# Optimization experiments

Measured on AMD Instinct MI355X. Metric: run time of the kernel, lower is better.

The kernel has to match this reference:

```python
import jax, jax.numpy as jnp
import numpy as np

N = 16384
D_IN = 1024
HID = [512, 512, 256]
N_PAIRS = 100000
N_CLS = 3


def setup_inputs() -> dict:
    key = jax.random.key(0)
    ks = jax.random.split(key, 16)
    x = jax.random.normal(ks[0], (N, D_IN), dtype=jnp.float32)
    adj = jax.random.uniform(ks[1], (N, N), dtype=jnp.float32) / N  # dense normalized adjacency
    tf_idx = jax.random.randint(ks[2], (N_PAIRS,), 0, N)
    gene_idx = jax.random.randint(ks[3], (N_PAIRS,), 0, N)
    # GCN layer weights
    W0 = jax.random.normal(ks[4], (D_IN, HID[0]), dtype=jnp.float32) / np.sqrt(D_IN)
    b0 = jnp.zeros((HID[0],), dtype=jnp.float32)
    W1 = jax.random.normal(ks[5], (HID[0], HID[1]), dtype=jnp.float32) / np.sqrt(HID[0])
    b1 = jnp.zeros((HID[1],), dtype=jnp.float32)
    W2 = jax.random.normal(ks[6], (HID[1], HID[2]), dtype=jnp.float32) / np.sqrt(HID[1])
    b2 = jnp.zeros((HID[2],), dtype=jnp.float32)
    # MLP head: Linear(2*256 -> 256), GELU, Linear(256 -> 3)
    Wh1 = jax.random.normal(ks[7], (2 * HID[2], HID[2]), dtype=jnp.float32) / np.sqrt(2 * HID[2])
    bh1 = jnp.zeros((HID[2],), dtype=jnp.float32)
    Wh2 = jax.random.normal(ks[8], (HID[2], N_CLS), dtype=jnp.float32) / np.sqrt(HID[2])
    bh2 = jnp.zeros((N_CLS,), dtype=jnp.float32)
    return {"x": x, "adj": adj, "tf_idx": tf_idx, "gene_idx": gene_idx,
            "W0": W0, "b0": b0, "W1": W1, "b1": b1, "W2": W2, "b2": b2,
            "Wh1": Wh1, "bh1": bh1, "Wh2": Wh2, "bh2": bh2}


def reference(x, adj, tf_idx, gene_idx, W0, b0, W1, b1, W2, b2, Wh1, bh1, Wh2, bh2):
    # GCNConv: out = adj @ (x @ W) + b; ReLU between layers (dropout off in eval)
    h = jax.nn.relu(adj @ (x @ W0) + b0)          # [N, 512]
    h = jax.nn.relu(adj @ (h @ W1) + b1)          # [N, 512]
    emb = adj @ (h @ W2) + b2                      # [N, 256]
    pair = jnp.concatenate([emb[tf_idx], emb[gene_idx]], axis=-1)  # [P, 512]
    hdn = jax.nn.gelu(pair @ Wh1 + bh1, approximate=False)          # [P, 256]
    logits = hdn @ Wh2 + bh2                                        # [P, 3]
    return logits
```

## Files before the change

### kernel.cpp

```cpp
#include <hip/hip_runtime.h>
#include <hip/hip_bf16.h>
#include <stdint.h>


using f32x4  = __attribute__((ext_vector_type(4))) float;
using bf16x8 = __attribute__((ext_vector_type(8))) __bf16;
using u16x8  = __attribute__((ext_vector_type(8))) unsigned short;
using u16x4  = __attribute__((ext_vector_type(4))) unsigned short;

static __device__ __forceinline__ unsigned short f2bf(float f) {
  unsigned u = __builtin_bit_cast(unsigned, f);
  u += 0x7FFFu + ((u >> 16) & 1u);
  return (unsigned short)(u >> 16);
}
static __device__ __forceinline__ float bf2f(unsigned short h) {
  unsigned u = ((unsigned)h) << 16;
  return __builtin_bit_cast(float, u);
}
static __device__ __forceinline__ void gload_lds16(const void* g, void* l) {
  __builtin_amdgcn_global_load_lds((__attribute__((address_space(1))) void*)(void*)g,
                                   (__attribute__((address_space(3))) void*)l,
                                   16, 0, 0);
}


__global__ void tcvt_kernel(const float* __restrict__ in,
                            unsigned short* __restrict__ outp, int K, int Nf) {
  int id = blockIdx.x * 256 + threadIdx.x;
  if (id >= K * Nf) return;
  int k = id % K, nf = id / K;
  outp[id] = f2bf(in[(size_t)k * Nf + nf]);
}

__global__ void cvt_bf16_kernel(const float* __restrict__ in,
                                unsigned short* __restrict__ outp, size_t n) {
  size_t i = ((size_t)blockIdx.x * blockDim.x + threadIdx.x) * 8;
  size_t stride = (size_t)gridDim.x * blockDim.x * 8;
  for (; i + 8 <= n; i += stride) {
    const float4* p = (const float4*)(in + i);
    float4 a = p[0], b = p[1];
    u16x8 v;
    v[0] = f2bf(a.x); v[1] = f2bf(a.y); v[2] = f2bf(a.z); v[3] = f2bf(a.w);
    v[4] = f2bf(b.x); v[5] = f2bf(b.y); v[6] = f2bf(b.z); v[7] = f2bf(b.w);
    *(u16x8*)(outp + i) = v;
  }
}

template <int NPART, bool RELU>
__global__ void reduceK_kernel(const float* __restrict__ Pp, const float* __restrict__ bias,
                               unsigned short* __restrict__ outp, int MN, int Nmask) {
  int i = (blockIdx.x * 256 + threadIdx.x) * 4;
  if (i >= MN) return;
  float4 s = *(const float4*)(Pp + i);
#pragma unroll
  for (int p = 1; p < NPART; ++p) {
    float4 v = *(const float4*)(Pp + (size_t)p * MN + i);
    s.x += v.x; s.y += v.y; s.z += v.z; s.w += v.w;
  }
  int col = i & Nmask;
  float r0 = s.x + bias[col + 0];
  float r1 = s.y + bias[col + 1];
  float r2 = s.z + bias[col + 2];
  float r3 = s.w + bias[col + 3];
  if (RELU) {
    r0 = fmaxf(r0, 0.0f); r1 = fmaxf(r1, 0.0f);
    r2 = fmaxf(r2, 0.0f); r3 = fmaxf(r3, 0.0f);
  }
  u16x4 o;
  o[0] = f2bf(r0); o[1] = f2bf(r1); o[2] = f2bf(r2); o[3] = f2bf(r3);
  *(u16x4*)(outp + i) = o;
}

template <int NI>
__global__ __launch_bounds__(512, 2)
void gemmA(const unsigned short* __restrict__ A, const unsigned short* __restrict__ Bt,
           float* __restrict__ Pp, int M, int N, int K) {
  constexpr int NL = 1 + NI;
  __shared__ __align__(16) unsigned short As[3 * 128 * 32];
  __shared__ __align__(16) unsigned short Bs[3 * NI * 128 * 32];
  const int t = threadIdx.x, l = t & 63, w = t >> 6;

  const int wg = (blockIdx.x & 7) * 32 + (blockIdx.x >> 3);
  const int kc = wg >> 7;
  const int mb = wg & 127;
  const int Klen = K >> 1;
  const int koff = kc * Klen;
  const int NT = Klen >> 5;
  const int fr = l & 15, fq = l >> 4;

  const unsigned short* AgR = A  + (size_t)(mb * 128 + (t >> 2)) * K + koff + (t & 3) * 8;
  const unsigned short* BgR = Bt + (size_t)(t >> 2) * K + koff + (t & 3) * 8;
  unsigned short* AsL = As + t * 8;
  unsigned short* BsL = Bs + t * 8;

#define STAGE_A(s, b)  gload_lds16(AgR + (size_t)(s) * 32, AsL + (b) * 4096);
#define STAGE_B(s, b)                                                         \
  _Pragma("unroll")                                                           \
  for (int j = 0; j < NI; ++j)                                                \
    gload_lds16(BgR + (size_t)(j * 128) * K + (size_t)(s) * 32,               \
                BsL + (b) * NI * 4096 + j * 4096);

  STAGE_A(0, 0) STAGE_B(0, 0)
  STAGE_A(1, 1) STAGE_B(1, 1)
  asm volatile("s_waitcnt vmcnt(%0)" :: "i"(NL) : "memory");
  __builtin_amdgcn_sched_barrier(0);
  __builtin_amdgcn_s_barrier();

  f32x4 acc[8][NI] = {};
  const int aoff = fr * 32 + fq * 8;
  const int boff = (w * (NI * 16) + fr) * 32 + fq * 8;

  int bb = 0, sb = 2;
  for (int tt = 0; tt < NT; ++tt) {
    const bool stg = (tt + 2) < NT;
    bf16x8 a03[4], a47[4], bf[NI];
#pragma unroll
    for (int mi = 0; mi < 4; ++mi)
      a03[mi] = *(const bf16x8*)&As[bb * 4096 + aoff + mi * 512];
#pragma unroll
    for (int ni = 0; ni < NI; ++ni)
      bf[ni] = *(const bf16x8*)&Bs[bb * NI * 4096 + boff + ni * 512];
#pragma unroll
    for (int mi = 0; mi < 4; ++mi)
      a47[mi] = *(const bf16x8*)&As[bb * 4096 + aoff + 2048 + mi * 512];
    if (stg) { STAGE_A(tt + 2, sb) }
    asm volatile("s_waitcnt lgkmcnt(4)" ::: "memory");
    __builtin_amdgcn_sched_barrier(0);
    __builtin_amdgcn_s_setprio(1);
#pragma unroll
    for (int mi = 0; mi < 4; ++mi)
#pragma unroll
      for (int ni = 0; ni < NI; ++ni)
        acc[mi][ni] = __builtin_amdgcn_mfma_f32_16x16x32_bf16(a03[mi], bf[ni],
                                                              acc[mi][ni], 0, 0, 0);
    __builtin_amdgcn_s_setprio(0);
    asm volatile("s_waitcnt lgkmcnt(0)" ::: "memory");
    __builtin_amdgcn_sched_barrier(0);
    __builtin_amdgcn_s_setprio(1);
#pragma unroll
    for (int mi = 0; mi < 4; ++mi)
#pragma unroll
      for (int ni = 0; ni < NI; ++ni)
        acc[mi + 4][ni] = __builtin_amdgcn_mfma_f32_16x16x32_bf16(a47[mi], bf[ni],
                                                                  acc[mi + 4][ni], 0, 0, 0);
    __builtin_amdgcn_s_setprio(0);
    if (stg) { STAGE_B(tt + 2, sb) }
    if (stg) {
      asm volatile("s_waitcnt vmcnt(%0)" :: "i"(NL) : "memory");
    } else {
      asm volatile("s_waitcnt vmcnt(0)" ::: "memory");
    }
    __builtin_amdgcn_sched_barrier(0);
    __builtin_amdgcn_s_barrier();
    bb = (bb == 2) ? 0 : bb + 1;
    sb = (sb == 2) ? 0 : sb + 1;
  }
#undef STAGE_B
#undef STAGE_A

  float* C = Pp + (size_t)kc * M * N;
  const int growb = mb * 128 + fq * 4;
  const int gcolb = w * (NI * 16) + fr;
#pragma unroll
  for (int mi = 0; mi < 8; ++mi) {
    int row = growb + mi * 16;
#pragma unroll
    for (int ni = 0; ni < NI; ++ni) {
      int col = gcolb + ni * 16;
      f32x4 v = acc[mi][ni];
#pragma unroll
      for (int r = 0; r < 4; ++r)
        C[(size_t)(row + r) * N + col] = v[r];
    }
  }
}

template <int EP, bool ABF16>
__global__ __launch_bounds__(256, 2)
void gemm_bt(const void* __restrict__ Av, const unsigned short* __restrict__ Bt,
             void* __restrict__ Cout, const float* __restrict__ bias,
             int M, int N, int K, int nbx, int Klen) {
  __shared__ __align__(16) unsigned short As[128 * 64];
  __shared__ __align__(16) unsigned short Bs[128 * 64];
  const int t = threadIdx.x;
  const int l = t & 63;
  const int w = t >> 6;

  int wg = blockIdx.x;
  const int cpx = gridDim.x >> 3;
  wg = (wg & 7) * cpx + (wg >> 3);
  const int mb = wg / nbx, nb = wg % nbx;
  const int kc = blockIdx.y;
  const int koff = kc * Klen;

  const int wr = w >> 1, wc = w & 1;
  f32x4 acc[4][4] = {};

  const int srow = w * 8 + (l >> 3);
  const int sk0  = 8 * ((l & 7) ^ (l >> 3));
  const unsigned short* Bg = Bt + (size_t)(nb * 128 + srow) * K + koff + sk0;
  unsigned short* BsL = Bs + w * 512 + l * 8;
  unsigned short* AsL = As + w * 512 + l * 8;

  const unsigned short* Ag16 = nullptr;
  const float* Ag32 = nullptr;
  unsigned short* AsWr = nullptr;
  int ak = 0, axm = 0;
  if constexpr (ABF16) {
    Ag16 = (const unsigned short*)Av + (size_t)(mb * 128 + srow) * K + koff + sk0;
  } else {
    const int ar = t >> 1;
    ak = (t & 1) * 32;
    axm = (ar & 7) << 3;
    Ag32 = (const float*)Av + (size_t)(mb * 128 + ar) * K + koff + ak;
    AsWr = As + ar * 64;
  }

  const int fr = l & 15, fq = l >> 4;
  const int rxor = (fr & 7) << 3;

  const int steps = Klen >> 6;
  for (int kb = 0; kb < steps; ++kb) {
#pragma unroll
    for (int i = 0; i < 4; ++i)
      gload_lds16(Bg + (size_t)i * 32 * K, BsL + i * 2048);
    Bg += 64;
    if constexpr (ABF16) {
#pragma unroll
      for (int i = 0; i < 4; ++i)
        gload_lds16(Ag16 + (size_t)i * 32 * K, AsL + i * 2048);
      Ag16 += 64;
    } else {
#pragma unroll
      for (int q = 0; q < 4; ++q) {
        float4 c0 = ((const float4*)Ag32)[q * 2];
        float4 c1 = ((const float4*)Ag32)[q * 2 + 1];
        u16x8 v;
        v[0] = f2bf(c0.x); v[1] = f2bf(c0.y); v[2] = f2bf(c0.z); v[3] = f2bf(c0.w);
        v[4] = f2bf(c1.x); v[5] = f2bf(c1.y); v[6] = f2bf(c1.z); v[7] = f2bf(c1.w);
        *(u16x8*)&AsWr[(ak + q * 8) ^ axm] = v;
      }
      Ag32 += 64;
    }
    __syncthreads();

    bf16x8 af[2][4], bfr[2][4];
#pragma unroll
    for (int kk = 0; kk < 2; ++kk) {
#pragma unroll
      for (int mi = 0; mi < 4; ++mi) {
        int arow = wr * 64 + mi * 16 + fr;
        af[kk][mi] = *(const bf16x8*)&As[arow * 64 + ((kk * 32 + fq * 8) ^ rxor)];
      }
#pragma unroll
      for (int ni = 0; ni < 4; ++ni) {
        int brow = wc * 64 + ni * 16 + fr;
        bfr[kk][ni] = *(const bf16x8*)&Bs[brow * 64 + ((kk * 32 + fq * 8) ^ rxor)];
      }
    }
#pragma unroll
    for (int kk = 0; kk < 2; ++kk)
#pragma unroll
      for (int mi = 0; mi < 4; ++mi)
#pragma unroll
        for (int ni = 0; ni < 4; ++ni)
          acc[mi][ni] = __builtin_amdgcn_mfma_f32_16x16x32_bf16(af[kk][mi], bfr[kk][ni],
                                                                acc[mi][ni], 0, 0, 0);
    __syncthreads();
  }

  const int r0 = fq * 4;
  const int c0 = fr;
  const int growb = mb * 128 + wr * 64 + r0;
  const int gcolb = nb * 128 + wc * 64 + c0;
  if constexpr (EP == 0) {
    unsigned short* Ct = (unsigned short*)Cout;
#pragma unroll
    for (int ni = 0; ni < 4; ++ni) {
      int col = gcolb + ni * 16;
#pragma unroll
      for (int mi = 0; mi < 4; ++mi) {
        int row = growb + mi * 16;
        f32x4 v = acc[mi][ni];
        u16x4 o;
        o[0] = f2bf(v[0]); o[1] = f2bf(v[1]); o[2] = f2bf(v[2]); o[3] = f2bf(v[3]);
        *(u16x4*)&Ct[(size_t)col * M + row] = o;
      }
    }
  } else if constexpr (EP == 1) {
    unsigned short* C = (unsigned short*)Cout;
#pragma unroll
    for (int ni = 0; ni < 4; ++ni) {
      int col = gcolb + ni * 16;
      float b = bias[col];
#pragma unroll
      for (int mi = 0; mi < 4; ++mi) {
        int row = growb + mi * 16;
        f32x4 v = acc[mi][ni];
#pragma unroll
        for (int r = 0; r < 4; ++r)
          C[(size_t)(row + r) * N + col] = f2bf(fmaxf(v[r] + b, 0.0f));
      }
    }
  } else {
    float* C = (float*)Cout + (size_t)kc * M * N;
#pragma unroll
    for (int ni = 0; ni < 4; ++ni) {
      int col = gcolb + ni * 16;
#pragma unroll
      for (int mi = 0; mi < 4; ++mi) {
        int row = growb + mi * 16;
        f32x4 v = acc[mi][ni];
#pragma unroll
        for (int r = 0; r < 4; ++r)
          C[(size_t)(row + r) * N + col] = v[r];
      }
    }
  }
}

__global__ __launch_bounds__(256, 2)
void head_kernel(const unsigned short* __restrict__ EMB, const int* __restrict__ tf,
                 const int* __restrict__ gi, const unsigned short* __restrict__ Wh1t,
                 const float* __restrict__ bh1, const float* __restrict__ Wh2,
                 const float* __restrict__ bh2, float* __restrict__ out, int P) {
  __shared__ __align__(16) union SU {
    struct { unsigned short As[64 * 64]; unsigned short Bs[256 * 64]; } s;
    unsigned short hdn[64 * 264];
  } u;
  __shared__ float wh2s[256 * 3];
  const int t = threadIdx.x, l = t & 63, w = t >> 6;
  const int pb = blockIdx.x;

  wh2s[t]       = Wh2[t];
  wh2s[t + 256] = Wh2[t + 256];
  wh2s[t + 512] = Wh2[t + 512];

  const int srow = w * 8 + (l >> 3);
  const int sk0  = 8 * ((l & 7) ^ (l >> 3));
  size_t tfo[2], gio[2];
#pragma unroll
  for (int i = 0; i < 2; ++i) {
    int p = pb * 64 + i * 32 + srow;
    if (p >= P) p = P - 1;
    tfo[i] = (size_t)tf[p] * 256;
    gio[i] = (size_t)gi[p] * 256;
  }
  const unsigned short* BgB = Wh1t + (size_t)srow * 512 + sk0;
  unsigned short* AsL = u.s.As + w * 512 + l * 8;
  unsigned short* BsL = u.s.Bs + w * 512 + l * 8;

  const int fr = l & 15, fq = l >> 4;
  const int rxor = (fr & 7) << 3;

  f32x4 acc[4][4] = {};
  for (int kb = 0; kb < 8; ++kb) {
    const int klo = (kb & 3) * 64 + sk0;
#pragma unroll
    for (int i = 0; i < 2; ++i)
      gload_lds16(EMB + ((kb < 4) ? tfo[i] : gio[i]) + klo, AsL + i * 2048);
#pragma unroll
    for (int i = 0; i < 8; ++i)
      gload_lds16(BgB + (size_t)i * 32 * 512 + kb * 64, BsL + i * 2048);
    __syncthreads();

    bf16x8 af[2][4], bfr[2][4];
#pragma unroll
    for (int kk = 0; kk < 2; ++kk) {
#pragma unroll
      for (int mi = 0; mi < 4; ++mi) {
        int arow = mi * 16 + fr;
        af[kk][mi] = *(const bf16x8*)&u.s.As[arow * 64 + ((kk * 32 + fq * 8) ^ rxor)];
      }
#pragma unroll
      for (int ni = 0; ni < 4; ++ni) {
        int brow = w * 64 + ni * 16 + fr;
        bfr[kk][ni] = *(const bf16x8*)&u.s.Bs[brow * 64 + ((kk * 32 + fq * 8) ^ rxor)];
      }
    }
#pragma unroll
    for (int kk = 0; kk < 2; ++kk)
#pragma unroll
      for (int mi = 0; mi < 4; ++mi)
#pragma unroll
        for (int ni = 0; ni < 4; ++ni)
          acc[mi][ni] = __builtin_amdgcn_mfma_f32_16x16x32_bf16(af[kk][mi], bfr[kk][ni],
                                                                acc[mi][ni], 0, 0, 0);
    __syncthreads();
  }

  const int r0 = fq * 4, c0 = fr;
#pragma unroll
  for (int ni = 0; ni < 4; ++ni) {
    int col = w * 64 + ni * 16 + c0;
    float b = bh1[col];
#pragma unroll
    for (int mi = 0; mi < 4; ++mi) {
      int row = mi * 16 + r0;
      f32x4 v = acc[mi][ni];
#pragma unroll
      for (int r = 0; r < 4; ++r) {
        float xv = v[r] + b;
        float g = 0.5f * xv * (1.0f + erff(xv * 0.70710678118f));
        u.hdn[(row + r) * 264 + col] = f2bf(g);
      }
    }
  }
  __syncthreads();

  const int pl = w * 16 + (l >> 2);
  const int pg = pb * 64 + pl;
  const int ks = (l & 3) * 64;
  float a0 = 0.f, a1 = 0.f, a2 = 0.f;
  const unsigned short* hr = u.hdn + pl * 264 + ks;
#pragma unroll
  for (int kq = 0; kq < 8; ++kq) {
    u16x8 hv = *(const u16x8*)(hr + kq * 8);
#pragma unroll
    for (int j = 0; j < 8; ++j) {
      float h = bf2f(hv[j]);
      int k = ks + kq * 8 + j;
      a0 = fmaf(h, wh2s[k * 3 + 0], a0);
      a1 = fmaf(h, wh2s[k * 3 + 1], a1);
      a2 = fmaf(h, wh2s[k * 3 + 2], a2);
    }
  }
  a0 += __shfl_xor(a0, 1); a0 += __shfl_xor(a0, 2);
  a1 += __shfl_xor(a1, 1); a1 += __shfl_xor(a1, 2);
  a2 += __shfl_xor(a2, 1); a2 += __shfl_xor(a2, 2);
  if ((l & 3) == 0 && pg < P) {
    out[(size_t)pg * 3 + 0] = a0 + bh2[0];
    out[(size_t)pg * 3 + 1] = a1 + bh2[1];
    out[(size_t)pg * 3 + 2] = a2 + bh2[2];
  }
}


extern "C" void kernel_launch(void* const* d_in, const int* in_sizes, int n_in,
                              void* d_out, int out_size, void* d_ws, size_t ws_size,
                              hipStream_t stream) {
  const float* x   = (const float*)d_in[0];
  const float* adj = (const float*)d_in[1];
  const int*   tf  = (const int*)d_in[2];
  const int*   gi  = (const int*)d_in[3];
  const float* W0  = (const float*)d_in[4];
  const float* b0  = (const float*)d_in[5];
  const float* W1  = (const float*)d_in[6];
  const float* b1  = (const float*)d_in[7];
  const float* W2  = (const float*)d_in[8];
  const float* b2  = (const float*)d_in[9];
  const float* Wh1 = (const float*)d_in[10];
  const float* bh1 = (const float*)d_in[11];
  const float* Wh2 = (const float*)d_in[12];
  const float* bh2 = (const float*)d_in[13];
  float* out = (float*)d_out;

  const int NN = 16384;
  const int P = in_sizes[2];

  char* ws = (char*)d_ws;
  size_t off = 0;
  auto alloc = [&](size_t bytes) -> char* {
    char* p = ws + off;
    off += (bytes + 255) & ~(size_t)255;
    return p;
  };
  unsigned short* W0t  = (unsigned short*)alloc((size_t)512 * 1024 * 2);
  unsigned short* W1t  = (unsigned short*)alloc((size_t)512 * 512 * 2);
  unsigned short* W2t  = (unsigned short*)alloc((size_t)256 * 512 * 2);
  unsigned short* Wh1t = (unsigned short*)alloc((size_t)256 * 512 * 2);
  unsigned short* Tt   = (unsigned short*)alloc((size_t)512 * NN * 2);
  unsigned short* H    = (unsigned short*)alloc((size_t)NN * 512 * 2);
  unsigned short* EMB  = (unsigned short*)alloc((size_t)NN * 256 * 2);
  float*          Pp   = (float*)alloc((size_t)2 * NN * 512 * 4);
  size_t base_end = off;

  bool useAdjB = false;
  unsigned short* adjb = nullptr;
  if (ws_size >= base_end + (size_t)NN * NN * 2) {
    adjb = (unsigned short*)alloc((size_t)NN * NN * 2);
    useAdjB = true;
  }

  tcvt_kernel<<<dim3((1024 * 512 + 255) / 256), 256, 0, stream>>>(W0, W0t, 1024, 512);
  tcvt_kernel<<<dim3((512 * 512 + 255) / 256), 256, 0, stream>>>(W1, W1t, 512, 512);
  tcvt_kernel<<<dim3((512 * 256 + 255) / 256), 256, 0, stream>>>(W2, W2t, 512, 256);
  tcvt_kernel<<<dim3((512 * 256 + 255) / 256), 256, 0, stream>>>(Wh1, Wh1t, 512, 256);
  if (useAdjB)
    cvt_bf16_kernel<<<4096, 256, 0, stream>>>(adj, adjb, (size_t)NN * NN);

  gemm_bt<0, false><<<dim3(512), 256, 0, stream>>>(x, W0t, Tt, nullptr,
                                                   NN, 512, 1024, 4, 1024);
  if (useAdjB) {
    gemmA<4><<<dim3(256), 512, 0, stream>>>(adjb, Tt, Pp, NN, 512, NN);
    reduceK_kernel<2, true><<<dim3(8192), 256, 0, stream>>>(Pp, b0, H, NN * 512, 511);
  } else {
    gemm_bt<1, false><<<dim3(512), 256, 0, stream>>>(adj, Tt, H, b0,
                                                     NN, 512, NN, 4, NN);
  }
  gemm_bt<0, true><<<dim3(512), 256, 0, stream>>>(H, W1t, Tt, nullptr,
                                                  NN, 512, 512, 4, 512);
  if (useAdjB) {
    gemmA<4><<<dim3(256), 512, 0, stream>>>(adjb, Tt, Pp, NN, 512, NN);
    reduceK_kernel<2, true><<<dim3(8192), 256, 0, stream>>>(Pp, b1, H, NN * 512, 511);
  } else {
    gemm_bt<1, false><<<dim3(512), 256, 0, stream>>>(adj, Tt, H, b1,
                                                     NN, 512, NN, 4, NN);
  }
  gemm_bt<0, true><<<dim3(256), 256, 0, stream>>>(H, W2t, Tt, nullptr,
                                                  NN, 256, 512, 2, 512);
  if (useAdjB) {
    gemmA<2><<<dim3(256), 512, 0, stream>>>(adjb, Tt, Pp, NN, 256, NN);
    reduceK_kernel<2, false><<<dim3(4096), 256, 0, stream>>>(Pp, b2, EMB, NN * 256, 255);
  } else {
    gemm_bt<3, false><<<dim3(256, 2), 256, 0, stream>>>(adj, Tt, Pp, nullptr,
                                                        NN, 256, NN, 2, NN / 2);
    reduceK_kernel<2, false><<<dim3(4096), 256, 0, stream>>>(Pp, b2, EMB, NN * 256, 255);
  }
  head_kernel<<<dim3((P + 63) / 64), 256, 0, stream>>>(EMB, tf, gi, Wh1t, bh1,
                                                       Wh2, bh2, out, P);
}
```

Baseline: 1.324 ms.

## Fuse fp32-to-bf16 adjacency conversion into the first adjacency GEMM

Removes the standalone pass that converts the dense adjacency to bf16. The first adjacency GEMM now reads fp32 adj directly, converts each tile in registers, writes it to LDS for the MFMA and also stores the bf16 copy for the later layers. This avoids reading the fp32 matrix twice (once in the convert pass, once in the GEMM). The cost is a new kernel with double buffering instead of triple, register-staged A loads, and launch bounds lowered to one block per SM, which may reduce latency hiding.

```diff
diff --git a/kernel.cpp b/kernel.cpp
--- a/kernel.cpp
+++ b/kernel.cpp
@@ -30,20 +30,6 @@
   if (id >= K * Nf) return;
   int k = id % K, nf = id / K;
   outp[id] = f2bf(in[(size_t)k * Nf + nf]);
-}
-
-__global__ void cvt_bf16_kernel(const float* __restrict__ in,
-                                unsigned short* __restrict__ outp, size_t n) {
-  size_t i = ((size_t)blockIdx.x * blockDim.x + threadIdx.x) * 8;
-  size_t stride = (size_t)gridDim.x * blockDim.x * 8;
-  for (; i + 8 <= n; i += stride) {
-    const float4* p = (const float4*)(in + i);
-    float4 a = p[0], b = p[1];
-    u16x8 v;
-    v[0] = f2bf(a.x); v[1] = f2bf(a.y); v[2] = f2bf(a.z); v[3] = f2bf(a.w);
-    v[4] = f2bf(b.x); v[5] = f2bf(b.y); v[6] = f2bf(b.z); v[7] = f2bf(b.w);
-    *(u16x8*)(outp + i) = v;
-  }
 }
 
 template <int NPART, bool RELU>
@@ -69,6 +55,115 @@
   u16x4 o;
   o[0] = f2bf(r0); o[1] = f2bf(r1); o[2] = f2bf(r2); o[3] = f2bf(r3);
   *(u16x4*)(outp + i) = o;
+}
+
+template <int NI>
+__global__ __launch_bounds__(512, 1)
+void gemmAF(const float* __restrict__ A, const unsigned short* __restrict__ Bt,
+            float* __restrict__ Pp, unsigned short* __restrict__ adjb,
+            int M, int N, int K) {
+  __shared__ __align__(16) unsigned short As[2 * 128 * 32];
+  __shared__ __align__(16) unsigned short Bs[2 * NI * 128 * 32];
+  const int t = threadIdx.x, l = t & 63, w = t >> 6;
+
+  const int wg = (blockIdx.x & 7) * 32 + (blockIdx.x >> 3);
+  const int kc = wg >> 7;
+  const int mb = wg & 127;
+  const int Klen = K >> 1;
+  const int koff = kc * Klen;
+  const int NT = Klen >> 5;
+  const int fr = l & 15, fq = l >> 4;
+
+  const int arow = t >> 2, ak0 = (t & 3) * 8;
+  const float* AgF = A + (size_t)(mb * 128 + arow) * K + koff + ak0;
+  unsigned short* AdjW = adjb + (size_t)(mb * 128 + arow) * K + koff + ak0;
+  const unsigned short* BgR = Bt + (size_t)(t >> 2) * K + koff + (t & 3) * 8;
+  unsigned short* BsL = Bs + t * 8;
+
+#define STAGE_B(s, b)                                                         \
+  _Pragma("unroll")                                                           \
+  for (int j = 0; j < NI; ++j)                                                \
+    gload_lds16(BgR + (size_t)(j * 128) * K + (size_t)(s) * 32,               \
+                BsL + (b) * NI * 4096 + j * 4096);
+
+  {
+    float4 r0 = ((const float4*)AgF)[0];
+    float4 r1 = ((const float4*)AgF)[1];
+    STAGE_B(0, 0)
+    u16x8 v;
+    v[0] = f2bf(r0.x); v[1] = f2bf(r0.y); v[2] = f2bf(r0.z); v[3] = f2bf(r0.w);
+    v[4] = f2bf(r1.x); v[5] = f2bf(r1.y); v[6] = f2bf(r1.z); v[7] = f2bf(r1.w);
+    *(u16x8*)&As[arow * 32 + ak0] = v;
+    *(u16x8*)AdjW = v;
+  }
+  __syncthreads();
+
+  f32x4 acc[8][NI] = {};
+  const int aoff = fr * 32 + fq * 8;
+  const int boff = (w * (NI * 16) + fr) * 32 + fq * 8;
+
+  for (int tt = 0; tt < NT; ++tt) {
+    const int bb = tt & 1;
+    bf16x8 a03[4], a47[4], bf[NI];
+#pragma unroll
+    for (int mi = 0; mi < 4; ++mi)
+      a03[mi] = *(const bf16x8*)&As[bb * 4096 + aoff + mi * 512];
+#pragma unroll
+    for (int ni = 0; ni < NI; ++ni)
+      bf[ni] = *(const bf16x8*)&Bs[bb * NI * 4096 + boff + ni * 512];
+#pragma unroll
+    for (int mi = 0; mi < 4; ++mi)
+      a47[mi] = *(const bf16x8*)&As[bb * 4096 + aoff + 2048 + mi * 512];
+
+    float4 r0, r1;
+    const bool stg = (tt + 1) < NT;
+    if (stg) {
+      r0 = ((const float4*)(AgF + (size_t)(tt + 1) * 32))[0];
+      r1 = ((const float4*)(AgF + (size_t)(tt + 1) * 32))[1];
+      STAGE_B(tt + 1, bb ^ 1)
+    }
+
+    __builtin_amdgcn_s_setprio(1);
+#pragma unroll
+    for (int mi = 0; mi < 4; ++mi)
+#pragma unroll
+      for (int ni = 0; ni < NI; ++ni)
+        acc[mi][ni] = __builtin_amdgcn_mfma_f32_16x16x32_bf16(a03[mi], bf[ni],
+                                                              acc[mi][ni], 0, 0, 0);
+#pragma unroll
+    for (int mi = 0; mi < 4; ++mi)
+#pragma unroll
+      for (int ni = 0; ni < NI; ++ni)
+        acc[mi + 4][ni] = __builtin_amdgcn_mfma_f32_16x16x32_bf16(a47[mi], bf[ni],
+                                                                  acc[mi + 4][ni], 0, 0, 0);
+    __builtin_amdgcn_s_setprio(0);
+
+    if (stg) {
+      u16x8 v;
+      v[0] = f2bf(r0.x); v[1] = f2bf(r0.y); v[2] = f2bf(r0.z); v[3] = f2bf(r0.w);
+      v[4] = f2bf(r1.x); v[5] = f2bf(r1.y); v[6] = f2bf(r1.z); v[7] = f2bf(r1.w);
+      *(u16x8*)&As[(bb ^ 1) * 4096 + arow * 32 + ak0] = v;
+      *(u16x8*)(AdjW + (size_t)(tt + 1) * 32) = v;
+    }
+    __syncthreads();
+  }
+#undef STAGE_B
+
+  float* C = Pp + (size_t)kc * M * N;
+  const int growb = mb * 128 + fq * 4;
+  const int gcolb = w * (NI * 16) + fr;
+#pragma unroll
+  for (int mi = 0; mi < 8; ++mi) {
+    int row = growb + mi * 16;
+#pragma unroll
+    for (int ni = 0; ni < NI; ++ni) {
+      int col = gcolb + ni * 16;
+      f32x4 v = acc[mi][ni];
+#pragma unroll
+      for (int r = 0; r < 4; ++r)
+        C[(size_t)(row + r) * N + col] = v[r];
+    }
+  }
 }
 
 template <int NI>
@@ -486,13 +581,11 @@
   tcvt_kernel<<<dim3((512 * 512 + 255) / 256), 256, 0, stream>>>(W1, W1t, 512, 512);
   tcvt_kernel<<<dim3((512 * 256 + 255) / 256), 256, 0, stream>>>(W2, W2t, 512, 256);
   tcvt_kernel<<<dim3((512 * 256 + 255) / 256), 256, 0, stream>>>(Wh1, Wh1t, 512, 256);
-  if (useAdjB)
-    cvt_bf16_kernel<<<4096, 256, 0, stream>>>(adj, adjb, (size_t)NN * NN);
 
   gemm_bt<0, false><<<dim3(512), 256, 0, stream>>>(x, W0t, Tt, nullptr,
                                                    NN, 512, 1024, 4, 1024);
   if (useAdjB) {
-    gemmA<4><<<dim3(256), 512, 0, stream>>>(adjb, Tt, Pp, NN, 512, NN);
+    gemmAF<4><<<dim3(256), 512, 0, stream>>>(adj, Tt, Pp, adjb, NN, 512, NN);
     reduceK_kernel<2, true><<<dim3(8192), 256, 0, stream>>>(Pp, b0, H, NN * 512, 511);
   } else {
     gemm_bt<1, false><<<dim3(512), 256, 0, stream>>>(adj, Tt, H, b0,
```

Result: no change. 1.336 ms (+0.9%).

## Split-K by four for 512-wide adjacency GEMMs, swizzle LDS, nontemporal partial stores

Applied to the files above, without the earlier changes.

The two 512-column adjacency GEMMs now split K four ways and launch 512 workgroups instead of 256, with a new block-to-(k-chunk, row-block) mapping and launch bounds relaxed to one block per SM. The LDS layout gets an XOR swizzle on the 16-byte column chunk to cut bank conflicts on fragment reads. Partial-sum stores become nontemporal. The extra split doubles the fp32 partial buffer and the reduce kernel's read traffic, trading it for more parallelism across CUs.

```diff
diff --git a/kernel.cpp b/kernel.cpp
--- a/kernel.cpp
+++ b/kernel.cpp
@@ -37,11 +37,11 @@
   size_t i = ((size_t)blockIdx.x * blockDim.x + threadIdx.x) * 8;
   size_t stride = (size_t)gridDim.x * blockDim.x * 8;
   for (; i + 8 <= n; i += stride) {
-    const float4* p = (const float4*)(in + i);
-    float4 a = p[0], b = p[1];
+    const f32x4* p = (const f32x4*)(in + i);
+    f32x4 a = p[0], b = p[1];
     u16x8 v;
-    v[0] = f2bf(a.x); v[1] = f2bf(a.y); v[2] = f2bf(a.z); v[3] = f2bf(a.w);
-    v[4] = f2bf(b.x); v[5] = f2bf(b.y); v[6] = f2bf(b.z); v[7] = f2bf(b.w);
+    v[0] = f2bf(a[0]); v[1] = f2bf(a[1]); v[2] = f2bf(a[2]); v[3] = f2bf(a[3]);
+    v[4] = f2bf(b[0]); v[5] = f2bf(b[1]); v[6] = f2bf(b[2]); v[7] = f2bf(b[3]);
     *(u16x8*)(outp + i) = v;
   }
 }
@@ -71,8 +71,20 @@
   *(u16x4*)(outp + i) = o;
 }
 
-template <int NI>
-__global__ __launch_bounds__(512, 2)
+template <int KDIV>
+static __device__ __forceinline__ void kmap(int b, int& kc, int& mb) {
+  if constexpr (KDIV == 4) {
+    kc = (b & 7) >> 1;
+    mb = ((b >> 3) << 1) | (b & 1);
+  } else {
+    const int wg = (b & 7) * 32 + (b >> 3);
+    kc = wg >> 7;
+    mb = wg & 127;
+  }
+}
+
+template <int NI, int KDIV>
+__global__ __launch_bounds__(512, 1)
 void gemmA(const unsigned short* __restrict__ A, const unsigned short* __restrict__ Bt,
            float* __restrict__ Pp, int M, int N, int K) {
   constexpr int NL = 1 + NI;
@@ -80,16 +92,17 @@
   __shared__ __align__(16) unsigned short Bs[3 * NI * 128 * 32];
   const int t = threadIdx.x, l = t & 63, w = t >> 6;
 
-  const int wg = (blockIdx.x & 7) * 32 + (blockIdx.x >> 3);
-  const int kc = wg >> 7;
-  const int mb = wg & 127;
-  const int Klen = K >> 1;
+  int kc, mb;
+  kmap<KDIV>(blockIdx.x, kc, mb);
+  const int Klen = K / KDIV;
   const int koff = kc * Klen;
   const int NT = Klen >> 5;
   const int fr = l & 15, fq = l >> 4;
-
-  const unsigned short* AgR = A  + (size_t)(mb * 128 + (t >> 2)) * K + koff + (t & 3) * 8;
-  const unsigned short* BgR = Bt + (size_t)(t >> 2) * K + koff + (t & 3) * 8;
+  const int sx = ((fr >> 1) & 3) << 3;
+  const int swz = (((t & 3) ^ ((t >> 3) & 3))) * 8;
+
+  const unsigned short* AgR = A  + (size_t)(mb * 128 + (t >> 2)) * K + koff + swz;
+  const unsigned short* BgR = Bt + (size_t)(t >> 2) * K + koff + swz;
   unsigned short* AsL = As + t * 8;
   unsigned short* BsL = Bs + t * 8;
 
@@ -107,8 +120,8 @@
   __builtin_amdgcn_s_barrier();
 
   f32x4 acc[8][NI] = {};
-  const int aoff = fr * 32 + fq * 8;
-  const int boff = (w * (NI * 16) + fr) * 32 + fq * 8;
+  const int aoff = fr * 32;
+  const int boff = (w * (NI * 16) + fr) * 32;
 
   int bb = 0, sb = 2;
   for (int tt = 0; tt < NT; ++tt) {
@@ -116,13 +129,13 @@
     bf16x8 a03[4], a47[4], bf[NI];
 #pragma unroll
     for (int mi = 0; mi < 4; ++mi)
-      a03[mi] = *(const bf16x8*)&As[bb * 4096 + aoff + mi * 512];
+      a03[mi] = *(const bf16x8*)&As[bb * 4096 + aoff + mi * 512 + ((fq * 8) ^ sx)];
 #pragma unroll
     for (int ni = 0; ni < NI; ++ni)
-      bf[ni] = *(const bf16x8*)&Bs[bb * NI * 4096 + boff + ni * 512];
+      bf[ni] = *(const bf16x8*)&Bs[bb * NI * 4096 + boff + ni * 512 + ((fq * 8) ^ sx)];
 #pragma unroll
     for (int mi = 0; mi < 4; ++mi)
-      a47[mi] = *(const bf16x8*)&As[bb * 4096 + aoff + 2048 + mi * 512];
+      a47[mi] = *(const bf16x8*)&As[bb * 4096 + aoff + 2048 + mi * 512 + ((fq * 8) ^ sx)];
     if (stg) { STAGE_A(tt + 2, sb) }
     asm volatile("s_waitcnt lgkmcnt(4)" ::: "memory");
     __builtin_amdgcn_sched_barrier(0);
@@ -170,7 +183,7 @@
       f32x4 v = acc[mi][ni];
 #pragma unroll
       for (int r = 0; r < 4; ++r)
-        C[(size_t)(row + r) * N + col] = v[r];
+        __builtin_nontemporal_store(v[r], &C[(size_t)(row + r) * N + col]);
     }
   }
 }
@@ -472,7 +485,7 @@
   unsigned short* Tt   = (unsigned short*)alloc((size_t)512 * NN * 2);
   unsigned short* H    = (unsigned short*)alloc((size_t)NN * 512 * 2);
   unsigned short* EMB  = (unsigned short*)alloc((size_t)NN * 256 * 2);
-  float*          Pp   = (float*)alloc((size_t)2 * NN * 512 * 4);
+  float*          Pp   = (float*)alloc((size_t)4 * NN * 512 * 4);
   size_t base_end = off;
 
   bool useAdjB = false;
@@ -492,8 +505,8 @@
   gemm_bt<0, false><<<dim3(512), 256, 0, stream>>>(x, W0t, Tt, nullptr,
                                                    NN, 512, 1024, 4, 1024);
   if (useAdjB) {
-    gemmA<4><<<dim3(256), 512, 0, stream>>>(adjb, Tt, Pp, NN, 512, NN);
-    reduceK_kernel<2, true><<<dim3(8192), 256, 0, stream>>>(Pp, b0, H, NN * 512, 511);
+    gemmA<4, 4><<<dim3(512), 512, 0, stream>>>(adjb, Tt, Pp, NN, 512, NN);
+    reduceK_kernel<4, true><<<dim3(8192), 256, 0, stream>>>(Pp, b0, H, NN * 512, 511);
   } else {
     gemm_bt<1, false><<<dim3(512), 256, 0, stream>>>(adj, Tt, H, b0,
                                                      NN, 512, NN, 4, NN);
@@ -501,8 +514,8 @@
   gemm_bt<0, true><<<dim3(512), 256, 0, stream>>>(H, W1t, Tt, nullptr,
                                                   NN, 512, 512, 4, 512);
   if (useAdjB) {
-    gemmA<4><<<dim3(256), 512, 0, stream>>>(adjb, Tt, Pp, NN, 512, NN);
-    reduceK_kernel<2, true><<<dim3(8192), 256, 0, stream>>>(Pp, b1, H, NN * 512, 511);
+    gemmA<4, 4><<<dim3(512), 512, 0, stream>>>(adjb, Tt, Pp, NN, 512, NN);
+    reduceK_kernel<4, true><<<dim3(8192), 256, 0, stream>>>(Pp, b1, H, NN * 512, 511);
   } else {
     gemm_bt<1, false><<<dim3(512), 256, 0, stream>>>(adj, Tt, H, b1,
                                                      NN, 512, NN, 4, NN);
@@ -510,7 +523,7 @@
   gemm_bt<0, true><<<dim3(256), 256, 0, stream>>>(H, W2t, Tt, nullptr,
                                                   NN, 256, 512, 2, 512);
   if (useAdjB) {
-    gemmA<2><<<dim3(256), 512, 0, stream>>>(adjb, Tt, Pp, NN, 256, NN);
+    gemmA<2, 2><<<dim3(256), 512, 0, stream>>>(adjb, Tt, Pp, NN, 256, NN);
     reduceK_kernel<2, false><<<dim3(4096), 256, 0, stream>>>(Pp, b2, EMB, NN * 256, 255);
   } else {
     gemm_bt<3, false><<<dim3(256, 2), 256, 0, stream>>>(adj, Tt, Pp, nullptr,
```

After: 1.356 ms. 1.02x slower.
